# Optimization experiments

Measured on AMD Instinct MI355X. Metric: run time of the kernel, lower is better.

Reference implementation:

```python
import jax, jax.numpy as jnp
import numpy as np

N, E, F_IN, F_HID, F_OUT = 100000, 1600000, 128, 128, 64


def setup_inputs() -> dict:
    key = jax.random.key(0)
    k = jax.random.split(key, 6)
    x = jax.random.normal(k[0], (N, F_IN), dtype=jnp.float32)
    edge_index = jax.random.randint(k[1], (2, E), 0, N, dtype=jnp.int32)
    # Glorot-ish init for the two GCNConv linear layers (+ bias, PyG default bias=True)
    W1 = jax.random.normal(k[2], (F_IN, F_HID), dtype=jnp.float32) * (1.0 / np.sqrt(F_IN))
    b1 = jnp.zeros((F_HID,), dtype=jnp.float32)
    W2 = jax.random.normal(k[3], (F_HID, F_OUT), dtype=jnp.float32) * (1.0 / np.sqrt(F_HID))
    b2 = jnp.zeros((F_OUT,), dtype=jnp.float32)
    return {"x": x, "edge_index": edge_index, "W1": W1, "b1": b1, "W2": W2, "b2": b2}


def reference(x, edge_index, W1, b1, W2, b2):
    n = x.shape[0]
    row, col = edge_index[0], edge_index[1]
    # gcn_norm with add_self_loops=True, edge_weight=None -> all-ones weights
    loop = jnp.arange(n, dtype=row.dtype)
    row = jnp.concatenate([row, loop])
    col = jnp.concatenate([col, loop])
    w = jnp.ones(row.shape[0], dtype=x.dtype)
    deg = jax.ops.segment_sum(w, col, num_segments=n)  # in-degree at targets
    dis = jnp.where(deg > 0, jax.lax.rsqrt(jnp.maximum(deg, 1.0)), 0.0)
    norm = dis[row] * w * dis[col]  # [E+N]

    def gcn_conv(h, W, b):
        h = h @ W                       # linear transform first (PyG order)
        msg = h[row] * norm[:, None]    # gather + scale, [E+N, d]
        return jax.ops.segment_sum(msg, col, num_segments=n) + b  # scatter-add

    h = jax.nn.relu(gcn_conv(x, W1, b1))
    # dropout is identity in eval mode
    return gcn_conv(h, W2, b2)
```

## Files before the change

kernel.cpp:

```cpp
#include <hip/hip_runtime.h>

#define F1 128
#define F2 64
#define BSH 9
#define BSZ 512

typedef unsigned int u32;
typedef unsigned short u16;
typedef __attribute__((ext_vector_type(8))) short bf16x8;
typedef __attribute__((ext_vector_type(4))) float f32x4;

__device__ __forceinline__ u32 bf16rne(float f) {
    u32 u = __float_as_uint(f);
    return (u + 0x7FFFu + ((u >> 16) & 1u)) >> 16;
}
__device__ __forceinline__ u32 pack2(float lo, float hi) {
    return bf16rne(lo) | (bf16rne(hi) << 16);
}
__device__ __forceinline__ float bflo(u32 u) { return __uint_as_float(u << 16); }
__device__ __forceinline__ float bfhi(u32 u) { return __uint_as_float(u & 0xFFFF0000u); }
__device__ __forceinline__ float bf1(u16 u) { return __uint_as_float((u32)u << 16); }


__global__ __launch_bounds__(256) void k_bhist(const int* __restrict__ colv,
                                               int* __restrict__ bucket_cnt, int E) {
    __shared__ int l[256];
    int t = threadIdx.x;
    l[t] = 0;
    __syncthreads();
    for (int e = blockIdx.x * blockDim.x + t; e < E; e += gridDim.x * blockDim.x)
        atomicAdd(&l[colv[e] >> BSH], 1);
    __syncthreads();
    if (l[t]) atomicAdd(&bucket_cnt[t], l[t]);
}

__global__ __launch_bounds__(256) void k_bscan(const int* __restrict__ bucket_cnt,
                                               int* __restrict__ bucket_base,
                                               int* __restrict__ bucket_cur,
                                               int* __restrict__ rowptr_last,
                                               int NB, int E) {
    __shared__ int s[256];
    int t = threadIdx.x;
    int v = (t < NB) ? bucket_cnt[t] : 0;
    s[t] = v;
    __syncthreads();
    for (int d = 1; d < 256; d <<= 1) {
        int u = (t >= d) ? s[t - d] : 0;
        __syncthreads();
        s[t] += u;
        __syncthreads();
    }
    int excl = s[t] - v;
    if (t < NB) { bucket_base[t] = excl; bucket_cur[t] = excl; }
    if (t == NB - 1) bucket_base[NB] = s[t];
    if (t == 0) *rowptr_last = E;
}

__global__ __launch_bounds__(256) void k_part(const int* __restrict__ rowv,
                                              const int* __restrict__ colv,
                                              int* __restrict__ bucket_cur,
                                              u32* __restrict__ ebuf, int E) {
    __shared__ int lcnt[256], lbase[256], loff[256];
    int t = threadIdx.x;
    lcnt[t] = 0; loff[t] = 0;
    __syncthreads();
    int rows[16], cols[16];
    int e0 = blockIdx.x * 4096;
#pragma unroll
    for (int it = 0; it < 16; it++) {
        int e = e0 + it * 256 + t;
        bool v = e < E;
        cols[it] = v ? colv[e] : -1;
        rows[it] = v ? rowv[e] : 0;
        if (v) atomicAdd(&lcnt[cols[it] >> BSH], 1);
    }
    __syncthreads();
    if (lcnt[t]) lbase[t] = atomicAdd(&bucket_cur[t], lcnt[t]);
    __syncthreads();
#pragma unroll
    for (int it = 0; it < 16; it++) {
        if (cols[it] >= 0) {
            int b = cols[it] >> BSH;
            int p = lbase[b] + atomicAdd(&loff[b], 1);
            ebuf[p] = ((u32)(cols[it] & (BSZ - 1)) << 17) | (u32)rows[it];
        }
    }
}

__global__ __launch_bounds__(512) void k_bfill(const u32* __restrict__ ebuf,
                                               const int* __restrict__ bucket_base,
                                               int* __restrict__ rowptr,
                                               float* __restrict__ dis,
                                               int* __restrict__ adj, int N) {
    __shared__ int cnt[BSZ], scn[BSZ], cur[BSZ];
    int t = threadIdx.x;
    int b = blockIdx.x;
    int e0 = bucket_base[b], e1 = bucket_base[b + 1];
    cnt[t] = 0;
    __syncthreads();
    for (int i = e0 + t; i < e1; i += BSZ)
        atomicAdd(&cnt[ebuf[i] >> 17], 1);
    __syncthreads();
    scn[t] = cnt[t];
    __syncthreads();
    for (int d = 1; d < BSZ; d <<= 1) {
        int u = (t >= d) ? scn[t - d] : 0;
        __syncthreads();
        scn[t] += u;
        __syncthreads();
    }
    int excl = scn[t] - cnt[t];
    cur[t] = excl;
    int node = (b << BSH) + t;
    if (node < N) {
        rowptr[node] = e0 + excl;
        dis[node] = rsqrtf((float)(cnt[t] + 1));
    }
    __syncthreads();
    for (int i = e0 + t; i < e1; i += BSZ) {
        u32 p = ebuf[i];
        int c = p >> 17;
        int r = (int)(p & 0x1FFFFu);
        int pos = atomicAdd(&cur[c], 1);
        adj[e0 + pos] = r;
    }
}


__global__ __launch_bounds__(256) void k_wprep(const float* __restrict__ W,
                                               uint4* __restrict__ wf, int NBc) {
    int t = blockIdx.x * 256 + threadIdx.x;
    int total = 4 * NBc * 64;
    if (t >= total) return;
    int lane = t & 63;
    int rem = t >> 6;
    int nb = rem % NBc;
    int kb = rem / NBc;
    int C = NBc * 16;
    int col = nb * 16 + (lane & 15);
    int krow = kb * 32 + (lane >> 4) * 8;
    u32 w[4];
#pragma unroll
    for (int p = 0; p < 4; p++) {
        float lo = W[(size_t)(krow + 2 * p) * C + col];
        float hi = W[(size_t)(krow + 2 * p + 1) * C + col];
        w[p] = pack2(lo, hi);
    }
    wf[t] = make_uint4(w[0], w[1], w[2], w[3]);
}


__global__ __launch_bounds__(256, 4) void k_gemm1(const float* __restrict__ x,
                                                  const uint4* __restrict__ w1f,
                                                  const float* __restrict__ dis,
                                                  u16* __restrict__ gb, int N) {
    int lane = threadIdx.x & 63;
    int wave = threadIdx.x >> 6;
    int m = lane & 15, quad = lane >> 4;
    int row0 = blockIdx.x * 64 + wave * 16;
    int arow = min(row0 + m, N - 1);
    const float* xr = x + (size_t)arow * F1 + quad * 8;
    bf16x8 a[4];
#pragma unroll
    for (int kb = 0; kb < 4; kb++) {
        float4 lo = *(const float4*)(xr + kb * 32);
        float4 hi = *(const float4*)(xr + kb * 32 + 4);
        a[kb][0] = (short)bf16rne(lo.x); a[kb][1] = (short)bf16rne(lo.y);
        a[kb][2] = (short)bf16rne(lo.z); a[kb][3] = (short)bf16rne(lo.w);
        a[kb][4] = (short)bf16rne(hi.x); a[kb][5] = (short)bf16rne(hi.y);
        a[kb][6] = (short)bf16rne(hi.z); a[kb][7] = (short)bf16rne(hi.w);
    }
    f32x4 acc[8];
#pragma unroll
    for (int nb = 0; nb < 8; nb++) acc[nb] = (f32x4)(0.0f);
#pragma unroll
    for (int nb = 0; nb < 8; nb++) {
#pragma unroll
        for (int kb = 0; kb < 4; kb++) {
            uint4 braw = w1f[(kb * 8 + nb) * 64 + lane];
            bf16x8 bf = *(bf16x8*)&braw;
            acc[nb] = __builtin_amdgcn_mfma_f32_16x16x32_bf16(a[kb], bf, acc[nb], 0, 0, 0);
        }
    }
    float dv[4];
    int rbase = row0 + quad * 4;
#pragma unroll
    for (int reg = 0; reg < 4; reg++) dv[reg] = dis[min(rbase + reg, N - 1)];
#pragma unroll
    for (int reg = 0; reg < 4; reg++) {
        int r = rbase + reg;
        if (r < N) {
            u16* gr = gb + (size_t)r * F1 + m;
#pragma unroll
            for (int nb = 0; nb < 8; nb++)
                gr[nb * 16] = (u16)bf16rne(acc[nb][reg] * dv[reg]);
        }
    }
}


__global__ __launch_bounds__(256) void k_agg1(const u32* __restrict__ g1,
                                              const int* __restrict__ rowptr,
                                              const int* __restrict__ adj,
                                              const float* __restrict__ dis,
                                              const float* __restrict__ b,
                                              u32* __restrict__ z, int N) {
    int node = __builtin_amdgcn_readfirstlane(blockIdx.x * 4 + (threadIdx.x >> 6));
    if (node >= N) return;
    int lane = threadIdx.x & 63;
    u32 sv = g1[(size_t)node * 64 + lane];
    float ax = bflo(sv), ay = bfhi(sv);
    int s = rowptr[node], e = rowptr[node + 1];
    int j = s;
    for (; j + 3 < e; j += 4) {
        int s0 = adj[j], s1 = adj[j + 1], s2 = adj[j + 2], s3 = adj[j + 3];
        u32 v0 = g1[(size_t)s0 * 64 + lane];
        u32 v1 = g1[(size_t)s1 * 64 + lane];
        u32 v2 = g1[(size_t)s2 * 64 + lane];
        u32 v3 = g1[(size_t)s3 * 64 + lane];
        ax += (bflo(v0) + bflo(v1)) + (bflo(v2) + bflo(v3));
        ay += (bfhi(v0) + bfhi(v1)) + (bfhi(v2) + bfhi(v3));
    }
    for (; j < e; j++) {
        u32 v = g1[(size_t)adj[j] * 64 + lane];
        ax += bflo(v); ay += bfhi(v);
    }
    float d = dis[node];
    float2 bb = ((const float2*)b)[lane];
    float ox = fmaxf(fmaf(d, ax, bb.x), 0.0f);
    float oy = fmaxf(fmaf(d, ay, bb.y), 0.0f);
    z[(size_t)node * 64 + lane] = pack2(ox, oy);
}


__global__ __launch_bounds__(256, 4) void k_gemm2(const u32* __restrict__ z,
                                                  const uint4* __restrict__ w2f,
                                                  const float* __restrict__ dis,
                                                  u16* __restrict__ gb, int N) {
    int lane = threadIdx.x & 63;
    int wave = threadIdx.x >> 6;
    int m = lane & 15, quad = lane >> 4;
    int row0 = blockIdx.x * 64 + wave * 16;
    int arow = min(row0 + m, N - 1);
    const u32* zr = z + (size_t)arow * 64 + quad * 4;
    bf16x8 a[4];
#pragma unroll
    for (int kb = 0; kb < 4; kb++) {
        uint4 za = *(const uint4*)(zr + kb * 16);
        a[kb] = *(bf16x8*)&za;
    }
    f32x4 acc[4];
#pragma unroll
    for (int nb = 0; nb < 4; nb++) acc[nb] = (f32x4)(0.0f);
#pragma unroll
    for (int nb = 0; nb < 4; nb++) {
#pragma unroll
        for (int kb = 0; kb < 4; kb++) {
            uint4 braw = w2f[(kb * 4 + nb) * 64 + lane];
            bf16x8 bf = *(bf16x8*)&braw;
            acc[nb] = __builtin_amdgcn_mfma_f32_16x16x32_bf16(a[kb], bf, acc[nb], 0, 0, 0);
        }
    }
    float dv[4];
    int rbase = row0 + quad * 4;
#pragma unroll
    for (int reg = 0; reg < 4; reg++) dv[reg] = dis[min(rbase + reg, N - 1)];
#pragma unroll
    for (int reg = 0; reg < 4; reg++) {
        int r = rbase + reg;
        if (r < N) {
            u16* gr = gb + (size_t)r * F2 + m;
#pragma unroll
            for (int nb = 0; nb < 4; nb++)
                gr[nb * 16] = (u16)bf16rne(acc[nb][reg] * dv[reg]);
        }
    }
}


__global__ __launch_bounds__(256) void k_agg2(const u16* __restrict__ g,
                                              const int* __restrict__ rowptr,
                                              const int* __restrict__ adj,
                                              const float* __restrict__ dis,
                                              const float* __restrict__ b,
                                              float* __restrict__ out, int N) {
    int node = __builtin_amdgcn_readfirstlane(blockIdx.x * 4 + (threadIdx.x >> 6));
    if (node >= N) return;
    int lane = threadIdx.x & 63;
    float acc = bf1(g[(size_t)node * F2 + lane]);
    int s = rowptr[node], e = rowptr[node + 1];
    int j = s;
    for (; j + 3 < e; j += 4) {
        int s0 = adj[j], s1 = adj[j + 1], s2 = adj[j + 2], s3 = adj[j + 3];
        float v0 = bf1(g[(size_t)s0 * F2 + lane]);
        float v1 = bf1(g[(size_t)s1 * F2 + lane]);
        float v2 = bf1(g[(size_t)s2 * F2 + lane]);
        float v3 = bf1(g[(size_t)s3 * F2 + lane]);
        acc += (v0 + v1) + (v2 + v3);
    }
    for (; j < e; j++) acc += bf1(g[(size_t)adj[j] * F2 + lane]);
    out[(size_t)node * F2 + lane] = fmaf(dis[node], acc, b[lane]);
}


extern "C" void kernel_launch(void* const* d_in, const int* in_sizes, int n_in,
                              void* d_out, int out_size, void* d_ws, size_t ws_size,
                              hipStream_t stream) {
    const float* x  = (const float*)d_in[0];
    const int*   ei = (const int*)d_in[1];
    const float* W1 = (const float*)d_in[2];
    const float* b1 = (const float*)d_in[3];
    const float* W2 = (const float*)d_in[4];
    const float* b2 = (const float*)d_in[5];
    float* out = (float*)d_out;

    const int N = in_sizes[0] / F1;
    const int E = in_sizes[1] / 2;
    const int NB = (N + BSZ - 1) >> BSH;
    const int* rowv = ei;
    const int* colv = ei + E;

    char* ws = (char*)d_ws;
    size_t off = 0;
    auto take = [&](size_t bytes) -> void* {
        void* p = ws + off;
        off += (bytes + 255) & ~(size_t)255;
        return p;
    };
    u16*   g1b     = (u16*)take((size_t)N * F1 * 2);
    u32*   zb      = (u32*)take((size_t)N * 64 * 4);
    u16*   g2b     = g1b;
    u32*   ebuf    = (u32*)g1b;
    float* dis     = (float*)take((size_t)N * 4);
    int*   rowptr  = (int*)take((size_t)(N + 1) * 4);
    int*   adj     = (int*)take((size_t)E * 4);
    uint4* w1f     = (uint4*)take(4 * 8 * 64 * 16);
    uint4* w2f     = (uint4*)take(4 * 4 * 64 * 16);
    int*   bucket_cnt  = (int*)take(256 * 4);
    int*   bucket_base = (int*)take(257 * 4);
    int*   bucket_cur  = (int*)take(256 * 4);

    hipMemsetAsync(bucket_cnt, 0, 256 * 4, stream);

    k_wprep<<<8, 256, 0, stream>>>(W1, w1f, 8);
    k_wprep<<<4, 256, 0, stream>>>(W2, w2f, 4);

    k_bhist<<<256, 256, 0, stream>>>(colv, bucket_cnt, E);
    k_bscan<<<1, 256, 0, stream>>>(bucket_cnt, bucket_base, bucket_cur, rowptr + N, NB, E);
    k_part<<<(E + 4095) / 4096, 256, 0, stream>>>(rowv, colv, bucket_cur, ebuf, E);
    k_bfill<<<NB, BSZ, 0, stream>>>(ebuf, bucket_base, rowptr, dis, adj, N);

    int gblocks = (N + 63) / 64;
    k_gemm1<<<gblocks, 256, 0, stream>>>(x, w1f, dis, g1b, N);
    k_agg1<<<(N + 3) / 4, 256, 0, stream>>>((const u32*)g1b, rowptr, adj, dis, b1, zb, N);
    k_gemm2<<<gblocks, 256, 0, stream>>>(zb, w2f, dis, g2b, N);
    k_agg2<<<(N + 3) / 4, 256, 0, stream>>>(g2b, rowptr, adj, dis, b2, out, N);
}
```

Measured before the change: 290.1 us.

## Vectorize aggregation gathers to 16-byte loads with multi-edge per wave and shuffle reduce

Both aggregation kernels now have each lane load a 16-byte chunk (8 bf16 features), so one wave processes several neighbor rows at once: 4 per load in agg1 and 8 in agg2. Partial sums are reduced with cross-lane XOR shuffles before one lane group writes the output with vector stores. The goal is fewer memory instructions and more memory-level parallelism per wave in the gather-bound phases, at the cost of extra shuffle work and idle lanes when a node has few edges. The two weight-prep launches are also merged into one kernel.

```diff
diff --git a/kernel.cpp b/kernel.cpp
--- a/kernel.cpp
+++ b/kernel.cpp
@@ -19,7 +19,13 @@
 }
 __device__ __forceinline__ float bflo(u32 u) { return __uint_as_float(u << 16); }
 __device__ __forceinline__ float bfhi(u32 u) { return __uint_as_float(u & 0xFFFF0000u); }
-__device__ __forceinline__ float bf1(u16 u) { return __uint_as_float((u32)u << 16); }
+
+__device__ __forceinline__ void acc8(float* ax, uint4 v) {
+    ax[0] += bflo(v.x); ax[1] += bfhi(v.x);
+    ax[2] += bflo(v.y); ax[3] += bfhi(v.y);
+    ax[4] += bflo(v.z); ax[5] += bfhi(v.z);
+    ax[6] += bflo(v.w); ax[7] += bfhi(v.w);
+}
 
 
 __global__ __launch_bounds__(256) void k_bhist(const int* __restrict__ colv,
@@ -127,11 +133,8 @@
 }
 
 
-__global__ __launch_bounds__(256) void k_wprep(const float* __restrict__ W,
-                                               uint4* __restrict__ wf, int NBc) {
-    int t = blockIdx.x * 256 + threadIdx.x;
-    int total = 4 * NBc * 64;
-    if (t >= total) return;
+__device__ __forceinline__ void wprep_do(const float* __restrict__ W,
+                                         uint4* __restrict__ wf, int NBc, int t) {
     int lane = t & 63;
     int rem = t >> 6;
     int nb = rem % NBc;
@@ -147,6 +150,15 @@
         w[p] = pack2(lo, hi);
     }
     wf[t] = make_uint4(w[0], w[1], w[2], w[3]);
+}
+
+__global__ __launch_bounds__(256) void k_wprep(const float* __restrict__ W1,
+                                               const float* __restrict__ W2,
+                                               uint4* __restrict__ w1f,
+                                               uint4* __restrict__ w2f) {
+    int blk = blockIdx.x;
+    if (blk < 8) wprep_do(W1, w1f, 8, blk * 256 + threadIdx.x);
+    else         wprep_do(W2, w2f, 4, (blk - 8) * 256 + threadIdx.x);
 }
 
 
@@ -199,37 +211,58 @@
 }
 
 
-__global__ __launch_bounds__(256) void k_agg1(const u32* __restrict__ g1,
+__global__ __launch_bounds__(256) void k_agg1(const uint4* __restrict__ g1,
                                               const int* __restrict__ rowptr,
                                               const int* __restrict__ adj,
                                               const float* __restrict__ dis,
                                               const float* __restrict__ b,
-                                              u32* __restrict__ z, int N) {
+                                              uint4* __restrict__ z, int N) {
     int node = __builtin_amdgcn_readfirstlane(blockIdx.x * 4 + (threadIdx.x >> 6));
     if (node >= N) return;
     int lane = threadIdx.x & 63;
-    u32 sv = g1[(size_t)node * 64 + lane];
-    float ax = bflo(sv), ay = bfhi(sv);
+    int grp = lane >> 4;
+    int sub = lane & 15;
+    float ax[8];
+#pragma unroll
+    for (int i = 0; i < 8; i++) ax[i] = 0.0f;
+    if (grp == 0) acc8(ax, g1[(size_t)node * 16 + sub]);
     int s = rowptr[node], e = rowptr[node + 1];
     int j = s;
-    for (; j + 3 < e; j += 4) {
-        int s0 = adj[j], s1 = adj[j + 1], s2 = adj[j + 2], s3 = adj[j + 3];
-        u32 v0 = g1[(size_t)s0 * 64 + lane];
-        u32 v1 = g1[(size_t)s1 * 64 + lane];
-        u32 v2 = g1[(size_t)s2 * 64 + lane];
-        u32 v3 = g1[(size_t)s3 * 64 + lane];
-        ax += (bflo(v0) + bflo(v1)) + (bflo(v2) + bflo(v3));
-        ay += (bfhi(v0) + bfhi(v1)) + (bfhi(v2) + bfhi(v3));
-    }
-    for (; j < e; j++) {
-        u32 v = g1[(size_t)adj[j] * 64 + lane];
-        ax += bflo(v); ay += bfhi(v);
-    }
-    float d = dis[node];
-    float2 bb = ((const float2*)b)[lane];
-    float ox = fmaxf(fmaf(d, ax, bb.x), 0.0f);
-    float oy = fmaxf(fmaf(d, ay, bb.y), 0.0f);
-    z[(size_t)node * 64 + lane] = pack2(ox, oy);
+    for (; j + 7 < e; j += 8) {
+        int s0 = adj[j + grp];
+        int s1 = adj[j + 4 + grp];
+        uint4 v0 = g1[(size_t)s0 * 16 + sub];
+        uint4 v1 = g1[(size_t)s1 * 16 + sub];
+        acc8(ax, v0);
+        acc8(ax, v1);
+    }
+    for (; j < e; j += 4) {
+        int idx = j + grp;
+        if (idx < e) acc8(ax, g1[(size_t)adj[idx] * 16 + sub]);
+    }
+#pragma unroll
+    for (int i = 0; i < 8; i++) {
+        ax[i] += __shfl_xor(ax[i], 16);
+        ax[i] += __shfl_xor(ax[i], 32);
+    }
+    if (grp == 0) {
+        float d = dis[node];
+        float4 b0 = *(const float4*)(b + 8 * sub);
+        float4 b1 = *(const float4*)(b + 8 * sub + 4);
+        float o[8];
+        o[0] = fmaxf(fmaf(d, ax[0], b0.x), 0.0f);
+        o[1] = fmaxf(fmaf(d, ax[1], b0.y), 0.0f);
+        o[2] = fmaxf(fmaf(d, ax[2], b0.z), 0.0f);
+        o[3] = fmaxf(fmaf(d, ax[3], b0.w), 0.0f);
+        o[4] = fmaxf(fmaf(d, ax[4], b1.x), 0.0f);
+        o[5] = fmaxf(fmaf(d, ax[5], b1.y), 0.0f);
+        o[6] = fmaxf(fmaf(d, ax[6], b1.z), 0.0f);
+        o[7] = fmaxf(fmaf(d, ax[7], b1.w), 0.0f);
+        uint4 ov;
+        ov.x = pack2(o[0], o[1]); ov.y = pack2(o[2], o[3]);
+        ov.z = pack2(o[4], o[5]); ov.w = pack2(o[6], o[7]);
+        z[(size_t)node * 16 + sub] = ov;
+    }
 }
 
 
@@ -278,7 +311,7 @@
 }
 
 
-__global__ __launch_bounds__(256) void k_agg2(const u16* __restrict__ g,
+__global__ __launch_bounds__(256) void k_agg2(const uint4* __restrict__ g,
                                               const int* __restrict__ rowptr,
                                               const int* __restrict__ adj,
                                               const float* __restrict__ dis,
@@ -287,19 +320,45 @@
     int node = __builtin_amdgcn_readfirstlane(blockIdx.x * 4 + (threadIdx.x >> 6));
     if (node >= N) return;
     int lane = threadIdx.x & 63;
-    float acc = bf1(g[(size_t)node * F2 + lane]);
+    int grp = lane >> 3;
+    int sub = lane & 7;
+    float ax[8];
+#pragma unroll
+    for (int i = 0; i < 8; i++) ax[i] = 0.0f;
+    if (grp == 0) acc8(ax, g[(size_t)node * 8 + sub]);
     int s = rowptr[node], e = rowptr[node + 1];
     int j = s;
-    for (; j + 3 < e; j += 4) {
-        int s0 = adj[j], s1 = adj[j + 1], s2 = adj[j + 2], s3 = adj[j + 3];
-        float v0 = bf1(g[(size_t)s0 * F2 + lane]);
-        float v1 = bf1(g[(size_t)s1 * F2 + lane]);
-        float v2 = bf1(g[(size_t)s2 * F2 + lane]);
-        float v3 = bf1(g[(size_t)s3 * F2 + lane]);
-        acc += (v0 + v1) + (v2 + v3);
-    }
-    for (; j < e; j++) acc += bf1(g[(size_t)adj[j] * F2 + lane]);
-    out[(size_t)node * F2 + lane] = fmaf(dis[node], acc, b[lane]);
+    for (; j + 15 < e; j += 16) {
+        int s0 = adj[j + grp];
+        int s1 = adj[j + 8 + grp];
+        uint4 v0 = g[(size_t)s0 * 8 + sub];
+        uint4 v1 = g[(size_t)s1 * 8 + sub];
+        acc8(ax, v0);
+        acc8(ax, v1);
+    }
+    for (; j < e; j += 8) {
+        int idx = j + grp;
+        if (idx < e) acc8(ax, g[(size_t)adj[idx] * 8 + sub]);
+    }
+#pragma unroll
+    for (int i = 0; i < 8; i++) {
+        ax[i] += __shfl_xor(ax[i], 8);
+        ax[i] += __shfl_xor(ax[i], 16);
+        ax[i] += __shfl_xor(ax[i], 32);
+    }
+    if (grp == 0) {
+        float d = dis[node];
+        float4 b0 = *(const float4*)(b + 8 * sub);
+        float4 b1 = *(const float4*)(b + 8 * sub + 4);
+        float4 o0, o1;
+        o0.x = fmaf(d, ax[0], b0.x); o0.y = fmaf(d, ax[1], b0.y);
+        o0.z = fmaf(d, ax[2], b0.z); o0.w = fmaf(d, ax[3], b0.w);
+        o1.x = fmaf(d, ax[4], b1.x); o1.y = fmaf(d, ax[5], b1.y);
+        o1.z = fmaf(d, ax[6], b1.z); o1.w = fmaf(d, ax[7], b1.w);
+        float4* op = (float4*)(out + (size_t)node * F2 + 8 * sub);
+        op[0] = o0;
+        op[1] = o1;
+    }
 }
 
 
@@ -342,8 +401,7 @@
 
     hipMemsetAsync(bucket_cnt, 0, 256 * 4, stream);
 
-    k_wprep<<<8, 256, 0, stream>>>(W1, w1f, 8);
-    k_wprep<<<4, 256, 0, stream>>>(W2, w2f, 4);
+    k_wprep<<<12, 256, 0, stream>>>(W1, W2, w1f, w2f);
 
     k_bhist<<<256, 256, 0, stream>>>(colv, bucket_cnt, E);
     k_bscan<<<1, 256, 0, stream>>>(bucket_cnt, bucket_base, bucket_cur, rowptr + N, NB, E);
@@ -352,7 +410,8 @@
 
     int gblocks = (N + 63) / 64;
     k_gemm1<<<gblocks, 256, 0, stream>>>(x, w1f, dis, g1b, N);
-    k_agg1<<<(N + 3) / 4, 256, 0, stream>>>((const u32*)g1b, rowptr, adj, dis, b1, zb, N);
+    k_agg1<<<(N + 3) / 4, 256, 0, stream>>>((const uint4*)g1b, rowptr, adj, dis, b1,
+                                            (uint4*)zb, N);
     k_gemm2<<<gblocks, 256, 0, stream>>>(zb, w2f, dis, g2b, N);
-    k_agg2<<<(N + 3) / 4, 256, 0, stream>>>(g2b, rowptr, adj, dis, b2, out, N);
-}
+    k_agg2<<<(N + 3) / 4, 256, 0, stream>>>((const uint4*)g2b, rowptr, adj, dis, b2, out, N);
+}
```

Result: no change. 286.2 us (-1.3%).
